# Kernel tuning notes

Measured on AMD Instinct MI355X. Metric: run time of the kernel, lower is better.

## Reference

```python
import jax, jax.numpy as jnp
import numpy as np

T, D, H, KEXP = 91, 256, 4, 4
DH = D // H
NA, NRG = 128, 1024
NEG = -1e10
SCALE = 2.0  # sqrt(head_num=4), faithful to the original (NOT sqrt(dh))


def _ln(x, g, b, eps=1e-5):
    m = jnp.mean(x, axis=-1, keepdims=True)
    v = jnp.mean((x - m) ** 2, axis=-1, keepdims=True)
    return (x - m) * jax.lax.rsqrt(v + eps) * g + b


def setup_inputs() -> dict:
    key = jax.random.key(0)
    ks = jax.random.split(key, 16)
    s = lambda fan_in: 1.0 / np.sqrt(fan_in)
    inp = {
        "agent": jax.random.normal(ks[0], (NA, T, D), jnp.float32),
        "rg": jax.random.normal(ks[1], (NRG, T, D), jnp.float32),
        "ln_x_g": jnp.ones((D,), jnp.float32),
        "ln_x_b": jnp.zeros((D,), jnp.float32),
        "wk": jax.random.uniform(ks[2], (D, D), jnp.float32, -s(D), s(D)),
        "bk": jnp.zeros((D,), jnp.float32),
        "wv": jax.random.uniform(ks[3], (D, D), jnp.float32, -s(D), s(D)),
        "bv": jnp.zeros((D,), jnp.float32),
        "wq": jax.random.uniform(ks[4], (D, D), jnp.float32, -s(D), s(D)),
        "bq": jnp.zeros((D,), jnp.float32),
        "q_scale": jnp.full((DH,), 0.001, jnp.float32),
        "wy": jax.random.uniform(ks[5], (D, D), jnp.float32, -s(D), s(D)),
        "by": jnp.zeros((D,), jnp.float32),
        "wf1": jax.random.uniform(ks[6], (D, KEXP * D), jnp.float32, -s(D), s(D)),
        "bf1": jnp.zeros((KEXP * D,), jnp.float32),
        "wf2": jax.random.uniform(ks[7], (KEXP * D, D), jnp.float32, -s(KEXP * D), s(KEXP * D)),
        "bf2": jnp.zeros((D,), jnp.float32),
        "ln_z_g": jnp.ones((D,), jnp.float32),
        "ln_z_b": jnp.zeros((D,), jnp.float32),
        "agent_rg_mask": jax.random.randint(ks[8], (T, NA, NRG), 0, 2).astype(bool),
        "padding_mask": jax.random.randint(ks[9], (T, NRG), 0, 2).astype(bool),
        "rg_valid_mask": jax.random.randint(ks[10], (T, NA), 0, 2).astype(bool),
    }
    return inp


def reference(agent, rg, ln_x_g, ln_x_b, wk, bk, wv, bv, wq, bq, q_scale,
              wy, by, wf1, bf1, wf2, bf2, ln_z_g, ln_z_b,
              agent_rg_mask, padding_mask, rg_valid_mask):
    agent_n = _ln(agent, ln_x_g, ln_x_b)   # (Na, T, D)
    rg_n = _ln(rg, ln_x_g, ln_x_b)         # (Nrg, T, D)

    K = jax.nn.relu(rg_n @ wk + bk).reshape(NRG, T, H, DH)
    V = jax.nn.relu(rg_n @ wv + bv).reshape(NRG, T, H, DH)
    Q = jax.nn.relu(agent_n @ wq + bq).reshape(NA, T, H, DH) * q_scale

    # energy: (T, H, Na, Nrg)
    energy = jnp.einsum("athd,rthd->thar", Q, K) / SCALE
    energy = jnp.where(agent_rg_mask[:, None, :, :], energy, NEG)
    energy = jnp.where(padding_mask[:, None, None, :], energy, NEG)
    energy = jnp.where(rg_valid_mask[:, None, :, None], energy, NEG)
    attn = jax.nn.softmax(energy, axis=-1)

    Y1 = jnp.einsum("thar,rthd->athd", attn, V).reshape(NA, T, D)
    Y2 = jax.nn.relu(Y1 @ wy + by)
    S = Y2 + agent_n
    F1 = jax.nn.relu(S @ wf1 + bf1)
    F2 = jax.nn.relu(F1 @ wf2 + bf2)
    Z = _ln(F2, ln_z_g, ln_z_b)

    Qp = jnp.transpose(Q, (1, 2, 0, 3))  # (T,H,Na,dh)
    Kp = jnp.transpose(K, (1, 2, 0, 3))
    Vp = jnp.transpose(V, (1, 2, 0, 3))
    return (Z, Qp, Kp, Vp)
```

## Files before the change

### kernel.cpp

```cpp
#include <hip/hip_runtime.h>

#define T_   91
#define D_   256
#define H_   4
#define DH_  64
#define NA_  128
#define NRG_ 1024
#define KEXP_ 4

typedef float f32x4 __attribute__((ext_vector_type(4)));
typedef short bf16x8 __attribute__((ext_vector_type(8)));

static constexpr float P_EPS = 1.3877787807814457e-17f;

__device__ inline ushort f2bf(float f) {
    union { float f; unsigned u; } v; v.f = f;
    unsigned r = (v.u + 0x7fffu + ((v.u >> 16) & 1u)) >> 16;
    return (ushort)r;
}
__device__ inline unsigned pk2(float a, float b) {
    return (unsigned)f2bf(a) | ((unsigned)f2bf(b) << 16);
}
__device__ inline float bf2f(ushort b) {
    union { unsigned u; float f; } v; v.u = ((unsigned)b) << 16;
    return v.f;
}

#define LN_BLOCKS 2912
#define PM_BLOCKS 2912
#define PW_BLOCKS 3072
#define KV_BLOCKS 5824

__global__ __launch_bounds__(256) void prep_all(
    const float* __restrict__ agent,
    const float* __restrict__ g, const float* __restrict__ b,
    const int* __restrict__ am, const int* __restrict__ pm,
    const int* __restrict__ vmk,
    const float* __restrict__ wk, const float* __restrict__ wv,
    const float* __restrict__ wq, const float* __restrict__ wy,
    const float* __restrict__ wf1, const float* __restrict__ wf2,
    ushort* __restrict__ agn, unsigned* __restrict__ cm,
    ushort* __restrict__ wkvt, ushort* __restrict__ wqt,
    ushort* __restrict__ wyt, ushort* __restrict__ wf1t,
    ushort* __restrict__ wf2t) {
    __shared__ int pmS[NRG_];
    int bid = blockIdx.x;
    if (bid < LN_BLOCKS) {
        int row = bid * 4 + (threadIdx.x >> 6);
        int lane = threadIdx.x & 63;
        f32x4 x = *(const f32x4*)(agent + (size_t)row * D_ + lane * 4);
        float s1 = x[0] + x[1] + x[2] + x[3];
        float s2 = x[0] * x[0] + x[1] * x[1] + x[2] * x[2] + x[3] * x[3];
#pragma unroll
        for (int off = 1; off < 64; off <<= 1) {
            s1 += __shfl_xor(s1, off);
            s2 += __shfl_xor(s2, off);
        }
        float mean = s1 * (1.0f / 256.0f);
        float var = s2 * (1.0f / 256.0f) - mean * mean;
        float rstd = rsqrtf(var + 1e-5f);
        f32x4 gv = *(const f32x4*)(g + lane * 4);
        f32x4 bv = *(const f32x4*)(b + lane * 4);
        float y0 = (x[0] - mean) * rstd * gv[0] + bv[0];
        float y1 = (x[1] - mean) * rstd * gv[1] + bv[1];
        float y2 = (x[2] - mean) * rstd * gv[2] + bv[2];
        float y3 = (x[3] - mean) * rstd * gv[3] + bv[3];
        *(uint2*)(agn + (size_t)row * D_ + lane * 4) =
            make_uint2(pk2(y0, y1), pk2(y2, y3));
    } else if (bid < LN_BLOCKS + PM_BLOCKS) {
        int base = (bid - LN_BLOCKS) * 4;
        int t = base / NA_;
        int w = threadIdx.x >> 6, lane = threadIdx.x & 63;
#pragma unroll
        for (int i = 0; i < 4; ++i)
            pmS[threadIdx.x + i * 256] = pm[(size_t)t * NRG_ + threadIdx.x + i * 256];
        __syncthreads();
        int idx = base + w;
        int a = idx & (NA_ - 1);
        int valid = vmk[t * NA_ + a];
        const int* amrow = am + (size_t)idx * NRG_;
#pragma unroll
        for (int c = 0; c < 16; ++c) {
            int r = c * 64 + lane;
            bool bit = valid && amrow[r] && pmS[r];
            unsigned long long msk = __ballot(bit);
            if (lane == 0) {
                cm[(size_t)idx * 32 + c * 2]     = (unsigned)msk;
                cm[(size_t)idx * 32 + c * 2 + 1] = (unsigned)(msk >> 32);
            }
        }
    } else {
        int idx = (bid - LN_BLOCKS - PM_BLOCKS) * 256 + threadIdx.x;
        if (idx < 131072) {
            const float* W = (idx < 65536) ? wk : wv;
            int li = idx & 65535;
            int n = li >> 8, k = li & 255;
            wkvt[idx] = f2bf(W[(size_t)k * 256 + n]);
        } else if (idx < 196608) {
            int li = idx - 131072;
            int n = li >> 8, k = li & 255;
            wqt[li] = f2bf(wq[(size_t)k * 256 + n]);
        } else if (idx < 262144) {
            int li = idx - 196608;
            int n = li >> 8, k = li & 255;
            wyt[li] = f2bf(wy[(size_t)k * 256 + n]);
        } else if (idx < 524288) {
            int li = idx - 262144;
            int n = li >> 8, k = li & 255;
            wf1t[li] = f2bf(wf1[(size_t)k * 1024 + n]);
        } else {
            int li = idx - 524288;
            int n = li >> 10, k = li & 1023;
            wf2t[li] = f2bf(wf2[(size_t)k * 256 + n]);
        }
    }
}

__global__ __launch_bounds__(512) void gemm_kvq(
    const float* __restrict__ rgf, const ushort* __restrict__ agn,
    const float* __restrict__ lng, const float* __restrict__ lnb,
    const ushort* __restrict__ wkvt, const ushort* __restrict__ wqt,
    const float* __restrict__ bk, const float* __restrict__ bv,
    const float* __restrict__ bq, const float* __restrict__ qs,
    float* __restrict__ Kp, float* __restrict__ Vp, float* __restrict__ Qp,
    ushort* __restrict__ Kb, ushort* __restrict__ Vtb, ushort* __restrict__ Qb) {
    __shared__ ushort Asf[64][264];
    __shared__ ushort Bs[128][72];
    float (*Et)[68] = (float(*)[68])&Asf[0][0];

    int bid = blockIdx.x;
    bool isQ = bid >= KV_BLOCKS;
    int bxi = 0, nh, t, rb = 0, a0 = 0;
    if (!isQ) {
        int chunk = bid >> 5, rem = bid & 31;
        int q = rem >> 3;
        int tidx = chunk * 8 + (rem & 7);
        bxi = q >> 1; nh = q & 1;
        t = tidx >> 4; rb = (tidx & 15) << 6;
    } else {
        int qid = bid - KV_BLOCKS;
        t = qid >> 2;
        int sub = qid & 3;
        a0 = (sub >> 1) << 6; nh = sub & 1;
    }
    int bnw = bxi * 256 + nh * 128;
    const ushort* Bt = isQ ? (wqt + (size_t)nh * 128 * 256) : (wkvt + (size_t)bnw * 256);

    int tid = threadIdx.x;
    int w = tid >> 6, lane = tid & 63;
    int wm = w >> 2, wn = w & 3;
    int l15 = lane & 15, l4 = lane >> 4;

    if (!isQ) {
        int row = tid >> 3, l8 = tid & 7;
        const float* ap = rgf + ((size_t)(rb + row) * T_ + t) * 256;
        f32x4 xr[8];
#pragma unroll
        for (int c = 0; c < 8; ++c) xr[c] = *(const f32x4*)(ap + l8 * 4 + c * 32);
        float s1 = 0.0f, s2 = 0.0f;
#pragma unroll
        for (int c = 0; c < 8; ++c)
#pragma unroll
            for (int r = 0; r < 4; ++r) { s1 += xr[c][r]; s2 += xr[c][r] * xr[c][r]; }
#pragma unroll
        for (int off = 1; off < 8; off <<= 1) {
            s1 += __shfl_xor(s1, off);
            s2 += __shfl_xor(s2, off);
        }
        float mean = s1 * (1.0f / 256.0f);
        float var = s2 * (1.0f / 256.0f) - mean * mean;
        float rstd = rsqrtf(var + 1e-5f);
#pragma unroll
        for (int c = 0; c < 8; ++c) {
            int col = l8 * 4 + c * 32;
            f32x4 g4 = *(const f32x4*)(lng + col);
            f32x4 b4 = *(const f32x4*)(lnb + col);
            float y0 = (xr[c][0] - mean) * rstd * g4[0] + b4[0];
            float y1 = (xr[c][1] - mean) * rstd * g4[1] + b4[1];
            float y2 = (xr[c][2] - mean) * rstd * g4[2] + b4[2];
            float y3 = (xr[c][3] - mean) * rstd * g4[3] + b4[3];
            *(uint2*)&Asf[row][col] = make_uint2(pk2(y0, y1), pk2(y2, y3));
        }
    } else {
#pragma unroll
        for (int i2 = 0; i2 < 4; ++i2) {
            int chunk = tid + i2 * 512;
            int row = chunk >> 5, c8 = (chunk & 31) * 8;
            *(bf16x8*)&Asf[row][c8] =
                *(const bf16x8*)(agn + ((size_t)(a0 + row) * T_ + t) * 256 + c8);
        }
    }

    f32x4 acc[2][2];
#pragma unroll
    for (int i = 0; i < 2; ++i)
#pragma unroll
        for (int j = 0; j < 2; ++j)
#pragma unroll
            for (int r = 0; r < 4; ++r) acc[i][j][r] = 0.0f;

    for (int k0 = 0; k0 < 256; k0 += 64) {
#pragma unroll
        for (int it = 0; it < 2; ++it) {
            int li = tid + it * 512;
            int row = li >> 3, c8 = (li & 7) * 8;
            *(bf16x8*)&Bs[row][c8] =
                *(const bf16x8*)(Bt + (size_t)row * 256 + k0 + c8);
        }
        __syncthreads();
#pragma unroll
        for (int kk = 0; kk < 2; ++kk) {
            bf16x8 af[2], bfr[2];
#pragma unroll
            for (int i = 0; i < 2; ++i)
                af[i] = *(const bf16x8*)&Asf[wm * 32 + i * 16 + l15][k0 + kk * 32 + l4 * 8];
#pragma unroll
            for (int j = 0; j < 2; ++j)
                bfr[j] = *(const bf16x8*)&Bs[wn * 32 + j * 16 + l15][kk * 32 + l4 * 8];
#pragma unroll
            for (int i = 0; i < 2; ++i)
#pragma unroll
                for (int j = 0; j < 2; ++j)
                    acc[i][j] = __builtin_amdgcn_mfma_f32_16x16x32_bf16(
                        af[i], bfr[j], acc[i][j], 0, 0, 0);
        }
        __syncthreads();
    }

    float v[2][2][4];
#pragma unroll
    for (int i = 0; i < 2; ++i)
#pragma unroll
        for (int j = 0; j < 2; ++j)
#pragma unroll
            for (int reg = 0; reg < 4; ++reg) {
                int nl = wn * 32 + j * 16 + l15;
                int np = nh * 128 + nl;
                float bs = isQ ? bq[np] : (bxi ? bv[np] : bk[np]);
                float x = fmaxf(acc[i][j][reg] + bs, 0.0f);
                if (isQ) x *= qs[np & 63];
                v[i][j][reg] = x;
            }

#pragma unroll 1
    for (int jq = 0; jq < 2; ++jq) {
        __syncthreads();
        if ((wn >> 1) == jq) {
#pragma unroll
            for (int i = 0; i < 2; ++i)
#pragma unroll
                for (int j = 0; j < 2; ++j)
#pragma unroll
                    for (int reg = 0; reg < 4; ++reg)
                        Et[wm * 32 + i * 16 + l4 * 4 + reg][(wn & 1) * 32 + j * 16 + l15]
                            = v[i][j][reg];
        }
        __syncthreads();
        int h = nh * 2 + jq;

        if (isQ) {
            size_t base = (((size_t)t * H_ + h) * NA_ + a0) * DH_;
#pragma unroll
            for (int it = 0; it < 2; ++it) {
                int slot = it * 512 + tid;
                int row = slot >> 4, c4 = (slot & 15) * 4;
                *(f32x4*)(Qp + base + row * 64 + c4) = *(f32x4*)&Et[row][c4];
                uint2 u = make_uint2(pk2(Et[row][c4] * 0.5f, Et[row][c4 + 1] * 0.5f),
                                     pk2(Et[row][c4 + 2] * 0.5f, Et[row][c4 + 3] * 0.5f));
                *(uint2*)(Qb + base + row * 64 + c4) = u;
            }
        } else {
            size_t base = (((size_t)t * H_ + h) * NRG_ + rb) * DH_;
            float* of = bxi ? Vp : Kp;
#pragma unroll
            for (int it = 0; it < 2; ++it) {
                int slot = it * 512 + tid;
                int row = slot >> 4, c4 = (slot & 15) * 4;
                *(f32x4*)(of + base + row * 64 + c4) = *(f32x4*)&Et[row][c4];
            }
            if (!bxi) {
#pragma unroll
                for (int it = 0; it < 2; ++it) {
                    int slot = it * 512 + tid;
                    int row = slot >> 4, c4 = (slot & 15) * 4;
                    uint2 u = make_uint2(pk2(Et[row][c4], Et[row][c4 + 1]),
                                         pk2(Et[row][c4 + 2], Et[row][c4 + 3]));
                    *(uint2*)(Kb + base + row * 64 + c4) = u;
                }
            }
        }
    }

    if (!isQ && bxi) {
#pragma unroll 1
        for (int jq = 0; jq < 2; ++jq) {
            __syncthreads();
            if ((wn >> 1) == jq) {
#pragma unroll
                for (int i = 0; i < 2; ++i)
#pragma unroll
                    for (int j = 0; j < 2; ++j)
#pragma unroll
                        for (int reg = 0; reg < 4; ++reg)
                            Et[(wn & 1) * 32 + j * 16 + l15]
                              [wm * 32 + i * 16 + l4 * 4 + reg] = v[i][j][reg];
            }
            __syncthreads();
            int h = nh * 2 + jq;
            size_t tb = ((size_t)t * H_ + h) * DH_ * NRG_;
#pragma unroll
            for (int it = 0; it < 2; ++it) {
                int slot = it * 512 + tid;
                int d = slot >> 4, r4 = (slot & 15) * 4;
                uint2 u = make_uint2(pk2(Et[d][r4], Et[d][r4 + 1]),
                                     pk2(Et[d][r4 + 2], Et[d][r4 + 3]));
                *(uint2*)(Vtb + tb + (size_t)d * NRG_ + rb + r4) = u;
            }
        }
    }
}

__global__ __launch_bounds__(512) void gemm_wide(
    const ushort* __restrict__ Ab, const ushort* __restrict__ Bt,
    const float* __restrict__ bias0, const float* __restrict__ bias1,
    const float* __restrict__ aux0, const ushort* __restrict__ residb,
    float* __restrict__ out0, ushort* __restrict__ out2,
    int N, int K, int mode) {
    __shared__ ushort smem[64 * 72 + 256 * 72];
    __shared__ float lnp[2][64][4];
    ushort (*As)[72] = (ushort(*)[72])smem;
    ushort (*Bs)[72] = (ushort(*)[72])(smem + 64 * 72);
    float (*Et)[68] = (float(*)[68])smem;

    int bxi = blockIdx.x, by = blockIdx.y;
    int bn = bxi * 256, bm = by * 64;

    int tid = threadIdx.x;
    int w = tid >> 6, lane = tid & 63;
    int wm = w >> 2, wn = w & 3;
    int l15 = lane & 15, l4 = lane >> 4;

    f32x4 acc[2][4];
#pragma unroll
    for (int i = 0; i < 2; ++i)
#pragma unroll
        for (int j = 0; j < 4; ++j)
#pragma unroll
            for (int r = 0; r < 4; ++r) acc[i][j][r] = 0.0f;

    for (int k0 = 0; k0 < K; k0 += 64) {
        {
            int row = tid >> 3, c8 = (tid & 7) * 8;
            *(bf16x8*)&As[row][c8] =
                *(const bf16x8*)(Ab + (size_t)(bm + row) * K + k0 + c8);
        }
#pragma unroll
        for (int it = 0; it < 4; ++it) {
            int li = tid + it * 512;
            int row = li >> 3, c8 = (li & 7) * 8;
            *(bf16x8*)&Bs[row][c8] =
                *(const bf16x8*)(Bt + (size_t)(bn + row) * K + k0 + c8);
        }
        __syncthreads();
#pragma unroll
        for (int kk = 0; kk < 2; ++kk) {
            bf16x8 af[2], bfr[4];
#pragma unroll
            for (int i = 0; i < 2; ++i)
                af[i] = *(const bf16x8*)&As[wm * 32 + i * 16 + l15][kk * 32 + l4 * 8];
#pragma unroll
            for (int j = 0; j < 4; ++j)
                bfr[j] = *(const bf16x8*)&Bs[wn * 64 + j * 16 + l15][kk * 32 + l4 * 8];
#pragma unroll
            for (int i = 0; i < 2; ++i)
#pragma unroll
                for (int j = 0; j < 4; ++j)
                    acc[i][j] = __builtin_amdgcn_mfma_f32_16x16x32_bf16(
                        af[i], bfr[j], acc[i][j], 0, 0, 0);
        }
        __syncthreads();
    }

    float v[2][4][4];
#pragma unroll
    for (int i = 0; i < 2; ++i)
#pragma unroll
        for (int j = 0; j < 4; ++j)
#pragma unroll
            for (int reg = 0; reg < 4; ++reg) {
                int nl = wn * 64 + j * 16 + l15;
                int rowl = wm * 32 + i * 16 + l4 * 4 + reg;
                float bs = (mode == 0) ? bias0[bn + nl] : bias0[nl];
                float x = fmaxf(acc[i][j][reg] + bs, 0.0f);
                if (mode == 3) x += bf2f(residb[(size_t)(bm + rowl) * 256 + nl]);
                v[i][j][reg] = x;
            }

    if (mode == 5) {
        float rs_[2][4], rq_[2][4];
#pragma unroll
        for (int i = 0; i < 2; ++i)
#pragma unroll
            for (int reg = 0; reg < 4; ++reg) {
                float s = 0.0f, q = 0.0f;
#pragma unroll
                for (int j = 0; j < 4; ++j) {
                    float x = v[i][j][reg];
                    s += x; q += x * x;
                }
#pragma unroll
                for (int off = 1; off < 16; off <<= 1) {
                    s += __shfl_xor(s, off);
                    q += __shfl_xor(q, off);
                }
                rs_[i][reg] = s; rq_[i][reg] = q;
            }
        if (l15 == 0) {
#pragma unroll
            for (int i = 0; i < 2; ++i)
#pragma unroll
                for (int reg = 0; reg < 4; ++reg) {
                    int row = wm * 32 + i * 16 + l4 * 4 + reg;
                    lnp[0][row][wn] = rs_[i][reg];
                    lnp[1][row][wn] = rq_[i][reg];
                }
        }
        __syncthreads();
#pragma unroll
        for (int i = 0; i < 2; ++i)
#pragma unroll
            for (int reg = 0; reg < 4; ++reg) {
                int row = wm * 32 + i * 16 + l4 * 4 + reg;
                float S1 = lnp[0][row][0] + lnp[0][row][1] + lnp[0][row][2] + lnp[0][row][3];
                float S2 = lnp[1][row][0] + lnp[1][row][1] + lnp[1][row][2] + lnp[1][row][3];
                float mean = S1 * (1.0f / 256.0f);
                float var = S2 * (1.0f / 256.0f) - mean * mean;
                float rstd = rsqrtf(var + 1e-5f);
#pragma unroll
                for (int j = 0; j < 4; ++j) {
                    int nl = wn * 64 + j * 16 + l15;
                    float z = (v[i][j][reg] - mean) * rstd * bias1[nl] + aux0[nl];
                    out0[(size_t)(bm + row) * 256 + nl] = z;
                }
            }
        return;
    }

#pragma unroll 1
    for (int jq = 0; jq < 4; ++jq) {
        __syncthreads();
        if (wn == jq) {
#pragma unroll
            for (int i = 0; i < 2; ++i)
#pragma unroll
                for (int j = 0; j < 4; ++j)
#pragma unroll
                    for (int reg = 0; reg < 4; ++reg)
                        Et[wm * 32 + i * 16 + l4 * 4 + reg][j * 16 + l15] = v[i][j][reg];
        }
        __syncthreads();
#pragma unroll
        for (int it = 0; it < 2; ++it) {
            int slot = it * 512 + tid;
            int row = slot >> 4, c4 = (slot & 15) * 4;
            uint2 u = make_uint2(pk2(Et[row][c4], Et[row][c4 + 1]),
                                 pk2(Et[row][c4 + 2], Et[row][c4 + 3]));
            *(uint2*)(out2 + (size_t)(bm + row) * N + bn + jq * 64 + c4) = u;
        }
    }
}

__global__ __launch_bounds__(512) void attn_flash(
    const ushort* __restrict__ Qb, const ushort* __restrict__ Kb,
    const ushort* __restrict__ Vtb, const unsigned* __restrict__ cm,
    ushort* __restrict__ Y1b) {
    int th = blockIdx.x;
    int t = th >> 2, h = th & 3;
    int tid = threadIdx.x;
    int w = tid >> 6, lane = tid & 63;
    int l15 = lane & 15, l4 = lane >> 4;

    __shared__ ushort Ks[2][64][72];
    __shared__ ushort Vts[2][64][72];
    __shared__ ushort Ps[128][72];
    __shared__ unsigned cmAll[128][33];

    bf16x8 qf[2];
#pragma unroll
    for (int kk = 0; kk < 2; ++kk)
        qf[kk] = *(const bf16x8*)(Qb + ((size_t)th * NA_ + w * 16 + l15) * DH_
                                  + kk * 32 + l4 * 8);

    {
        const uint4* src = (const uint4*)(cm + (size_t)t * NA_ * 32 + tid * 8);
        uint4 c0 = src[0], c1 = src[1];
        int a = tid >> 2, wd = (tid & 3) * 8;
        cmAll[a][wd + 0] = c0.x; cmAll[a][wd + 1] = c0.y;
        cmAll[a][wd + 2] = c0.z; cmAll[a][wd + 3] = c0.w;
        cmAll[a][wd + 4] = c1.x; cmAll[a][wd + 5] = c1.y;
        cmAll[a][wd + 6] = c1.z; cmAll[a][wd + 7] = c1.w;
    }

    int srow = tid >> 3, sc8 = (tid & 7) * 8;
    const ushort* Kbase = Kb + (size_t)th * NRG_ * DH_;
    const ushort* Vbase = Vtb + (size_t)th * DH_ * NRG_;
    bf16x8 kreg = *(const bf16x8*)(Kbase + (size_t)srow * DH_ + sc8);
    bf16x8 vreg = *(const bf16x8*)(Vbase + (size_t)srow * NRG_ + sc8);
    *(bf16x8*)&Ks[0][srow][sc8] = kreg;
    *(bf16x8*)&Vts[0][srow][sc8] = vreg;
    __syncthreads();

    f32x4 o[4];
    float rsum[4] = {0.0f, 0.0f, 0.0f, 0.0f};
#pragma unroll
    for (int ds = 0; ds < 4; ++ds)
#pragma unroll
        for (int r = 0; r < 4; ++r) o[ds][r] = 0.0f;

    for (int rt = 0; rt < 16; ++rt) {
        int cur = rt & 1;
        if (rt < 15) {
            int r0n = (rt + 1) * 64;
            kreg = *(const bf16x8*)(Kbase + (size_t)(r0n + srow) * DH_ + sc8);
            vreg = *(const bf16x8*)(Vbase + (size_t)srow * NRG_ + r0n + sc8);
        }

        f32x4 e[4];
#pragma unroll
        for (int rs = 0; rs < 4; ++rs) {
#pragma unroll
            for (int r = 0; r < 4; ++r) e[rs][r] = 0.0f;
#pragma unroll
            for (int kk = 0; kk < 2; ++kk) {
                bf16x8 kf = *(const bf16x8*)&Ks[cur][rs * 16 + l15][kk * 32 + l4 * 8];
                e[rs] = __builtin_amdgcn_mfma_f32_16x16x32_bf16(qf[kk], kf, e[rs], 0, 0, 0);
            }
        }

#pragma unroll
        for (int reg = 0; reg < 4; ++reg) {
            int a_loc = w * 16 + l4 * 4 + reg;
            unsigned w0 = cmAll[a_loc][rt * 2], w1 = cmAll[a_loc][rt * 2 + 1];
#pragma unroll
            for (int rs = 0; rs < 4; ++rs) {
                unsigned wd = (rs & 2) ? w1 : w0;
                int bit = (wd >> ((rs & 1) * 16 + l15)) & 1;
                float p = bit ? __expf(e[rs][reg]) : P_EPS;
                rsum[reg] += p;
                Ps[a_loc][rs * 16 + l15] = f2bf(p);
            }
        }

#pragma unroll
        for (int rc = 0; rc < 2; ++rc) {
            bf16x8 pa = *(const bf16x8*)&Ps[w * 16 + l15][rc * 32 + l4 * 8];
#pragma unroll
            for (int ds = 0; ds < 4; ++ds) {
                bf16x8 vf = *(const bf16x8*)&Vts[cur][ds * 16 + l15][rc * 32 + l4 * 8];
                o[ds] = __builtin_amdgcn_mfma_f32_16x16x32_bf16(pa, vf, o[ds], 0, 0, 0);
            }
        }

        if (rt < 15) {
            *(bf16x8*)&Ks[cur ^ 1][srow][sc8] = kreg;
            *(bf16x8*)&Vts[cur ^ 1][srow][sc8] = vreg;
            __syncthreads();
        }
    }

#pragma unroll
    for (int off = 1; off < 16; off <<= 1)
#pragma unroll
        for (int reg = 0; reg < 4; ++reg)
            rsum[reg] += __shfl_xor(rsum[reg], off);
    float rinv[4];
#pragma unroll
    for (int reg = 0; reg < 4; ++reg) rinv[reg] = 1.0f / rsum[reg];

#pragma unroll
    for (int ds = 0; ds < 4; ++ds)
#pragma unroll
        for (int reg = 0; reg < 4; ++reg) {
            int a_g = w * 16 + l4 * 4 + reg;
            int d = ds * 16 + l15;
            Y1b[((size_t)a_g * T_ + t) * D_ + h * DH_ + d] = f2bf(o[ds][reg] * rinv[reg]);
        }
}

extern "C" void kernel_launch(void* const* d_in, const int* in_sizes, int n_in,
                              void* d_out, int out_size, void* d_ws, size_t ws_size,
                              hipStream_t stream) {
    const float* agent   = (const float*)d_in[0];
    const float* rg      = (const float*)d_in[1];
    const float* ln_x_g  = (const float*)d_in[2];
    const float* ln_x_b  = (const float*)d_in[3];
    const float* wk      = (const float*)d_in[4];
    const float* bk      = (const float*)d_in[5];
    const float* wv      = (const float*)d_in[6];
    const float* bv      = (const float*)d_in[7];
    const float* wq      = (const float*)d_in[8];
    const float* bq      = (const float*)d_in[9];
    const float* q_scale = (const float*)d_in[10];
    const float* wy      = (const float*)d_in[11];
    const float* by      = (const float*)d_in[12];
    const float* wf1     = (const float*)d_in[13];
    const float* bf1     = (const float*)d_in[14];
    const float* wf2     = (const float*)d_in[15];
    const float* bf2     = (const float*)d_in[16];
    const float* ln_z_g  = (const float*)d_in[17];
    const float* ln_z_b  = (const float*)d_in[18];
    const int*   am      = (const int*)d_in[19];
    const int*   pm      = (const int*)d_in[20];
    const int*   vmk     = (const int*)d_in[21];

    float* Z  = (float*)d_out;
    float* Qp = Z + (size_t)NA_ * T_ * D_;
    float* Kp = Qp + (size_t)NA_ * T_ * D_;
    float* Vp = Kp + (size_t)NRG_ * T_ * D_;

    char* p = (char*)d_ws;
    ushort* agn_b = (ushort*)p;   p += (size_t)NA_ * T_ * D_ * 2;
    ushort* wkvt  = (ushort*)p;   p += (size_t)512 * 256 * 2;
    ushort* wqt   = (ushort*)p;   p += (size_t)256 * 256 * 2;
    ushort* wyt   = (ushort*)p;   p += (size_t)256 * 256 * 2;
    ushort* wf1t  = (ushort*)p;   p += (size_t)1024 * 256 * 2;
    ushort* wf2t  = (ushort*)p;   p += (size_t)256 * 1024 * 2;
    unsigned* cm  = (unsigned*)p; p += (size_t)T_ * NA_ * 32 * 4;
    ushort* Kb    = (ushort*)p;   p += (size_t)T_ * H_ * NRG_ * DH_ * 2;
    ushort* Vtb   = (ushort*)p;   p += (size_t)T_ * H_ * NRG_ * DH_ * 2;
    ushort* Qb    = (ushort*)p;   p += (size_t)T_ * H_ * NA_ * DH_ * 2;
    ushort* Y1b   = (ushort*)p;   p += (size_t)NA_ * T_ * D_ * 2;
    ushort* Sb    = (ushort*)p;   p += (size_t)NA_ * T_ * D_ * 2;
    ushort* F1b   = (ushort*)p;   p += (size_t)NA_ * T_ * D_ * KEXP_ * 2;

    prep_all<<<dim3(LN_BLOCKS + PM_BLOCKS + PW_BLOCKS), dim3(256), 0, stream>>>(
        agent, ln_x_g, ln_x_b, am, pm, vmk,
        wk, wv, wq, wy, wf1, wf2,
        agn_b, cm, wkvt, wqt, wyt, wf1t, wf2t);

    gemm_kvq<<<dim3(KV_BLOCKS + T_ * 4), dim3(512), 0, stream>>>(
        rg, agn_b, ln_x_g, ln_x_b, wkvt, wqt, bk, bv, bq, q_scale,
        Kp, Vp, Qp, Kb, Vtb, Qb);

    attn_flash<<<dim3(T_ * H_), dim3(512), 0, stream>>>(Qb, Kb, Vtb, cm, Y1b);

    gemm_wide<<<dim3(1, NA_ * T_ / 64), dim3(512), 0, stream>>>(
        Y1b, wyt, by, nullptr, nullptr, agn_b,
        nullptr, Sb, 256, 256, 3);

    gemm_wide<<<dim3(4, NA_ * T_ / 64), dim3(512), 0, stream>>>(
        Sb, wf1t, bf1, nullptr, nullptr, nullptr,
        nullptr, F1b, 1024, 256, 0);

    gemm_wide<<<dim3(1, NA_ * T_ / 64), dim3(512), 0, stream>>>(
        F1b, wf2t, bf2, ln_z_g, ln_z_b, nullptr,
        Z, nullptr, 256, 1024, 5);
}
```

Before: 252.8 us.

## Stream A tiles per k-chunk in gemm_kvq to shrink LDS and raise occupancy

The full 64x256 A tile is no longer staged in shared memory. Each k-chunk now loads and normalizes only its own 64x64 slice. LDS shrinks from about 52KB to 27KB and launch bounds ask for higher occupancy. The V transpose epilogue is folded into the first pass through a separate transposed bf16 buffer, which removes one pair of syncs. The cost is re-reading rg rows from global memory twice (once for the stats, once per chunk) and exposing load latency inside the k-loop.

```diff
diff --git a/kernel.cpp b/kernel.cpp
--- a/kernel.cpp
+++ b/kernel.cpp
@@ -116,7 +116,7 @@
     }
 }
 
-__global__ __launch_bounds__(512) void gemm_kvq(
+__global__ __launch_bounds__(512, 8) void gemm_kvq(
     const float* __restrict__ rgf, const ushort* __restrict__ agn,
     const float* __restrict__ lng, const float* __restrict__ lnb,
     const ushort* __restrict__ wkvt, const ushort* __restrict__ wqt,
@@ -124,9 +124,11 @@
     const float* __restrict__ bq, const float* __restrict__ qs,
     float* __restrict__ Kp, float* __restrict__ Vp, float* __restrict__ Qp,
     ushort* __restrict__ Kb, ushort* __restrict__ Vtb, ushort* __restrict__ Qb) {
-    __shared__ ushort Asf[64][264];
-    __shared__ ushort Bs[128][72];
-    float (*Et)[68] = (float(*)[68])&Asf[0][0];
+    __shared__ char smem[64 * 72 * 2 + 128 * 72 * 2];
+    ushort (*As)[72] = (ushort(*)[72])smem;
+    ushort (*Bs)[72] = (ushort(*)[72])(smem + 64 * 72 * 2);
+    float (*Et)[68] = (float(*)[68])smem;
+    ushort (*Etr)[72] = (ushort(*)[72])(smem + 17408);
 
     int bid = blockIdx.x;
     bool isQ = bid >= KV_BLOCKS;
@@ -150,45 +152,30 @@
     int w = tid >> 6, lane = tid & 63;
     int wm = w >> 2, wn = w & 3;
     int l15 = lane & 15, l4 = lane >> 4;
-
+    int arow = tid >> 3, l8 = tid & 7;
+
+    float mean = 0.0f, rstd = 0.0f;
+    const float* ap = nullptr;
+    const ushort* aq = nullptr;
     if (!isQ) {
-        int row = tid >> 3, l8 = tid & 7;
-        const float* ap = rgf + ((size_t)(rb + row) * T_ + t) * 256;
-        f32x4 xr[8];
-#pragma unroll
-        for (int c = 0; c < 8; ++c) xr[c] = *(const f32x4*)(ap + l8 * 4 + c * 32);
+        ap = rgf + ((size_t)(rb + arow) * T_ + t) * 256;
         float s1 = 0.0f, s2 = 0.0f;
 #pragma unroll
-        for (int c = 0; c < 8; ++c)
-#pragma unroll
-            for (int r = 0; r < 4; ++r) { s1 += xr[c][r]; s2 += xr[c][r] * xr[c][r]; }
+        for (int c = 0; c < 8; ++c) {
+            f32x4 x = *(const f32x4*)(ap + l8 * 4 + c * 32);
+            s1 += x[0] + x[1] + x[2] + x[3];
+            s2 += x[0] * x[0] + x[1] * x[1] + x[2] * x[2] + x[3] * x[3];
+        }
 #pragma unroll
         for (int off = 1; off < 8; off <<= 1) {
             s1 += __shfl_xor(s1, off);
             s2 += __shfl_xor(s2, off);
         }
-        float mean = s1 * (1.0f / 256.0f);
+        mean = s1 * (1.0f / 256.0f);
         float var = s2 * (1.0f / 256.0f) - mean * mean;
-        float rstd = rsqrtf(var + 1e-5f);
-#pragma unroll
-        for (int c = 0; c < 8; ++c) {
-            int col = l8 * 4 + c * 32;
-            f32x4 g4 = *(const f32x4*)(lng + col);
-            f32x4 b4 = *(const f32x4*)(lnb + col);
-            float y0 = (xr[c][0] - mean) * rstd * g4[0] + b4[0];
-            float y1 = (xr[c][1] - mean) * rstd * g4[1] + b4[1];
-            float y2 = (xr[c][2] - mean) * rstd * g4[2] + b4[2];
-            float y3 = (xr[c][3] - mean) * rstd * g4[3] + b4[3];
-            *(uint2*)&Asf[row][col] = make_uint2(pk2(y0, y1), pk2(y2, y3));
-        }
+        rstd = rsqrtf(var + 1e-5f);
     } else {
-#pragma unroll
-        for (int i2 = 0; i2 < 4; ++i2) {
-            int chunk = tid + i2 * 512;
-            int row = chunk >> 5, c8 = (chunk & 31) * 8;
-            *(bf16x8*)&Asf[row][c8] =
-                *(const bf16x8*)(agn + ((size_t)(a0 + row) * T_ + t) * 256 + c8);
-        }
+        aq = agn + ((size_t)(a0 + arow) * T_ + t) * 256;
     }
 
     f32x4 acc[2][2];
@@ -200,6 +187,24 @@
             for (int r = 0; r < 4; ++r) acc[i][j][r] = 0.0f;
 
     for (int k0 = 0; k0 < 256; k0 += 64) {
+        if (!isQ) {
+#pragma unroll
+            for (int cc = 0; cc < 2; ++cc) {
+                int col = l8 * 4 + (k0 >> 5) * 32 + cc * 32;
+                f32x4 x = *(const f32x4*)(ap + col);
+                f32x4 g4 = *(const f32x4*)(lng + col);
+                f32x4 b4 = *(const f32x4*)(lnb + col);
+                float y0 = (x[0] - mean) * rstd * g4[0] + b4[0];
+                float y1 = (x[1] - mean) * rstd * g4[1] + b4[1];
+                float y2 = (x[2] - mean) * rstd * g4[2] + b4[2];
+                float y3 = (x[3] - mean) * rstd * g4[3] + b4[3];
+                *(uint2*)&As[arow][l8 * 4 + cc * 32] =
+                    make_uint2(pk2(y0, y1), pk2(y2, y3));
+            }
+        } else {
+            *(bf16x8*)&As[arow][l8 * 8] =
+                *(const bf16x8*)(aq + l8 * 8 + (k0 >> 6) * 64);
+        }
 #pragma unroll
         for (int it = 0; it < 2; ++it) {
             int li = tid + it * 512;
@@ -213,7 +218,7 @@
             bf16x8 af[2], bfr[2];
 #pragma unroll
             for (int i = 0; i < 2; ++i)
-                af[i] = *(const bf16x8*)&Asf[wm * 32 + i * 16 + l15][k0 + kk * 32 + l4 * 8];
+                af[i] = *(const bf16x8*)&As[wm * 32 + i * 16 + l15][kk * 32 + l4 * 8];
 #pragma unroll
             for (int j = 0; j < 2; ++j)
                 bfr[j] = *(const bf16x8*)&Bs[wn * 32 + j * 16 + l15][kk * 32 + l4 * 8];
@@ -249,11 +254,18 @@
 #pragma unroll
             for (int i = 0; i < 2; ++i)
 #pragma unroll
-                for (int j = 0; j < 2; ++j)
+                for (int j = 0; j < 2; ++j) {
+                    int colL = (wn & 1) * 32 + j * 16 + l15;
+                    int rowB = wm * 32 + i * 16 + l4 * 4;
 #pragma unroll
                     for (int reg = 0; reg < 4; ++reg)
-                        Et[wm * 32 + i * 16 + l4 * 4 + reg][(wn & 1) * 32 + j * 16 + l15]
-                            = v[i][j][reg];
+                        Et[rowB + reg][colL] = v[i][j][reg];
+                    if (!isQ && bxi) {
+                        *(uint2*)&Etr[colL][rowB] =
+                            make_uint2(pk2(v[i][j][0], v[i][j][1]),
+                                       pk2(v[i][j][2], v[i][j][3]));
+                    }
+                }
         }
         __syncthreads();
         int h = nh * 2 + jq;
@@ -269,52 +281,27 @@
                                      pk2(Et[row][c4 + 2] * 0.5f, Et[row][c4 + 3] * 0.5f));
                 *(uint2*)(Qb + base + row * 64 + c4) = u;
             }
-        } else {
+        } else if (!bxi) {
             size_t base = (((size_t)t * H_ + h) * NRG_ + rb) * DH_;
-            float* of = bxi ? Vp : Kp;
 #pragma unroll
             for (int it = 0; it < 2; ++it) {
                 int slot = it * 512 + tid;
                 int row = slot >> 4, c4 = (slot & 15) * 4;
-                *(f32x4*)(of + base + row * 64 + c4) = *(f32x4*)&Et[row][c4];
-            }
-            if (!bxi) {
-#pragma unroll
-                for (int it = 0; it < 2; ++it) {
-                    int slot = it * 512 + tid;
-                    int row = slot >> 4, c4 = (slot & 15) * 4;
-                    uint2 u = make_uint2(pk2(Et[row][c4], Et[row][c4 + 1]),
-                                         pk2(Et[row][c4 + 2], Et[row][c4 + 3]));
-                    *(uint2*)(Kb + base + row * 64 + c4) = u;
-                }
-            }
-        }
-    }
-
-    if (!isQ && bxi) {
-#pragma unroll 1
-        for (int jq = 0; jq < 2; ++jq) {
-            __syncthreads();
-            if ((wn >> 1) == jq) {
-#pragma unroll
-                for (int i = 0; i < 2; ++i)
-#pragma unroll
-                    for (int j = 0; j < 2; ++j)
-#pragma unroll
-                        for (int reg = 0; reg < 4; ++reg)
-                            Et[(wn & 1) * 32 + j * 16 + l15]
-                              [wm * 32 + i * 16 + l4 * 4 + reg] = v[i][j][reg];
-            }
-            __syncthreads();
-            int h = nh * 2 + jq;
+                *(f32x4*)(Kp + base + row * 64 + c4) = *(f32x4*)&Et[row][c4];
+                uint2 u = make_uint2(pk2(Et[row][c4], Et[row][c4 + 1]),
+                                     pk2(Et[row][c4 + 2], Et[row][c4 + 3]));
+                *(uint2*)(Kb + base + row * 64 + c4) = u;
+            }
+        } else {
+            size_t base = (((size_t)t * H_ + h) * NRG_ + rb) * DH_;
             size_t tb = ((size_t)t * H_ + h) * DH_ * NRG_;
 #pragma unroll
             for (int it = 0; it < 2; ++it) {
                 int slot = it * 512 + tid;
-                int d = slot >> 4, r4 = (slot & 15) * 4;
-                uint2 u = make_uint2(pk2(Et[d][r4], Et[d][r4 + 1]),
-                                     pk2(Et[d][r4 + 2], Et[d][r4 + 3]));
-                *(uint2*)(Vtb + tb + (size_t)d * NRG_ + rb + r4) = u;
+                int row = slot >> 4, c4 = (slot & 15) * 4;
+                *(f32x4*)(Vp + base + row * 64 + c4) = *(f32x4*)&Et[row][c4];
+                *(uint2*)(Vtb + tb + (size_t)row * NRG_ + rb + c4) =
+                    *(uint2*)&Etr[row][c4];
             }
         }
     }
```

Result: slower. 268.5 us (+6.2%).
